# Kernel tuning notes

Hardware: AMD Instinct MI355X
Metric: run time of the kernel (lower is better)

## Reference

```python
import jax, jax.numpy as jnp
import numpy as np

B, N, F, E, D = 2, 50000, 128, 800000, 4


def setup_inputs() -> dict:
    key = jax.random.key(0)
    ks = jax.random.split(key, 6)
    X = jax.random.normal(ks[0], (B, N, F), dtype=jnp.float32)
    u_val = jax.random.normal(ks[1], (E, D), dtype=jnp.float32)
    u_rows = jax.random.randint(ks[2], (E,), 0, N, dtype=jnp.int32)
    u_cols = jax.random.randint(ks[3], (E,), 0, N, dtype=jnp.int32)
    mu = jax.random.uniform(ks[4], (1, D), minval=-0.05, maxval=0.05, dtype=jnp.float32)
    # sigma kept away from 0 so sigma^2 in the denominator is numerically sane
    sigma = jax.random.uniform(ks[5], (1, D), minval=0.5, maxval=1.5, dtype=jnp.float32)
    return {"X": X, "u_val": u_val, "u_rows": u_rows, "u_cols": u_cols,
            "mu": mu, "sigma": sigma, "u_shape": N}


def reference(X, u_val, u_rows, u_cols, mu, sigma, u_shape):
    n = u_shape  # python int, static
    # per-edge Gaussian kernel log-weight: -0.5 * sum_d (u-mu)^2 / (sigma^2+eps)
    w = -0.5 * jnp.sum(jnp.square(u_val - mu) / (jnp.square(sigma) + 1e-14), axis=1)  # [E]
    # sparse (segment) softmax over rows == tf.sparse.softmax on reordered SparseTensor
    m = jax.ops.segment_max(w, u_rows, num_segments=n)          # [N]
    e = jnp.exp(w - m[u_rows])                                  # [E]
    s = jax.ops.segment_sum(e, u_rows, num_segments=n)          # [N]
    sm = e / s[u_rows]                                          # [E]
    # sparse-dense matmul: D[b,i,f] = sum_{edges e: row=i} sm_e * X[b, col_e, f]
    Xt = jnp.transpose(X, (1, 0, 2))                            # [N,B,F]
    msg = sm[:, None, None] * Xt[u_cols]                        # [E,B,F]
    Dn = jax.ops.segment_sum(msg, u_rows, num_segments=n)       # [N,B,F]
    return jnp.transpose(Dn, (1, 0, 2))                         # [B,N,F]
```

## Files before the change

kernel.cpp:

```cpp
#include <hip/hip_runtime.h>

constexpr int Bc = 2;
constexpr int Fc = 128;
constexpr int F4 = Fc / 4;
constexpr int ROWS_PER_BLOCK = 4;
constexpr int EPT = 8;
constexpr int BIN_EDGES = 256 * EPT;

typedef float vfloat4 __attribute__((ext_vector_type(4)));

__device__ __forceinline__ unsigned short f2bf(float f) {
    unsigned u = __float_as_uint(f);
    unsigned r = (u + 0x7FFFu + ((u >> 16) & 1u)) >> 16;
    return (unsigned short)r;
}
__device__ __forceinline__ float bf2f(unsigned short h) {
    return __uint_as_float(((unsigned)h) << 16);
}
__device__ __forceinline__ void nt_store4(float4 v, float4* p) {
    vfloat4 q = {v.x, v.y, v.z, v.w};
    __builtin_nontemporal_store(q, (vfloat4*)p);
}

__global__ __launch_bounds__(256) void prep_kernel(const float4* __restrict__ uval,
                                                   const float* __restrict__ mu,
                                                   const float* __restrict__ sigma,
                                                   const int* __restrict__ rows,
                                                   const int* __restrict__ cols,
                                                   int2* __restrict__ bucket_buf,
                                                   int* __restrict__ bucket_cursor,
                                                   const float4* __restrict__ X4,
                                                   ushort4* __restrict__ Xb,
                                                   int E, int N, int cap, int nbuk,
                                                   int nbin) {
    __shared__ int hist[256];
    __shared__ int excl[256];
    __shared__ int fill[256];
    __shared__ int chunkb[256];
    __shared__ int sh[256];
    __shared__ int2 staged[BIN_EDGES];

    int t = threadIdx.x;

    if (blockIdx.x >= nbin) {
        long idx = (long)(blockIdx.x - nbin) * 256 + t;
        long tot = (long)Bc * N * F4;
        if (idx < tot) {
            int b  = (int)(idx / ((long)N * F4));
            int nt_ = (int)(idx - (long)b * N * F4);
            int n  = nt_ >> 5;
            int f4 = nt_ & 31;
            float4 v = X4[(size_t)b * N * F4 + nt_];
            ushort4 o;
            o.x = f2bf(v.x); o.y = f2bf(v.y); o.z = f2bf(v.z); o.w = f2bf(v.w);
            Xb[(size_t)n * (Bc * F4) + b * F4 + f4] = o;
        }
        return;
    }

    hist[t] = 0;
    float m0 = mu[0], m1 = mu[1], m2 = mu[2], m3 = mu[3];
    float i0 = 1.0f / (sigma[0] * sigma[0] + 1e-14f);
    float i1 = 1.0f / (sigma[1] * sigma[1] + 1e-14f);
    float i2 = 1.0f / (sigma[2] * sigma[2] + 1e-14f);
    float i3 = 1.0f / (sigma[3] * sigma[3] + 1e-14f);
    __syncthreads();

    int e0 = blockIdx.x * BIN_EDGES;
    int meta_r[EPT];
    float ev_r[EPT];
    int buk_r[EPT];
    #pragma unroll
    for (int it = 0; it < EPT; ++it) {
        int e = e0 + it * 256 + t;
        if (e < E) {
            int r = rows[e];
            int c = cols[e];
            float4 u = uval[e];
            float d0 = u.x - m0, d1 = u.y - m1, d2 = u.z - m2, d3 = u.w - m3;
            float w = -0.5f * (d0 * d0 * i0 + d1 * d1 * i1 + d2 * d2 * i2 + d3 * d3 * i3);
            ev_r[it]   = expf(w);
            meta_r[it] = (r << 16) | c;
            buk_r[it]  = r >> 8;
            atomicAdd(&hist[buk_r[it]], 1);
        } else {
            buk_r[it] = -1;
        }
    }
    __syncthreads();

    int v = hist[t];
    sh[t] = v;
    __syncthreads();
    for (int off = 1; off < 256; off <<= 1) {
        int a = (t >= off) ? sh[t - off] : 0;
        __syncthreads();
        sh[t] += a;
        __syncthreads();
    }
    excl[t] = sh[t] - v;
    fill[t] = sh[t] - v;

    if (t < nbuk && v > 0) chunkb[t] = atomicAdd(&bucket_cursor[t], v);
    __syncthreads();

    #pragma unroll
    for (int it = 0; it < EPT; ++it) {
        if (buk_r[it] >= 0) {
            int rk = atomicAdd(&fill[buk_r[it]], 1);
            staged[rk] = make_int2(meta_r[it], __float_as_int(ev_r[it]));
        }
    }
    __syncthreads();

    int nst = min(BIN_EDGES, E - e0);
    for (int k = t; k < nst; k += 256) {
        int2 x = staged[k];
        int buk = ((unsigned)x.x) >> 24;
        int rel = chunkb[buk] + (k - excl[buk]);
        if (rel < cap)
            bucket_buf[(size_t)buk * cap + rel] = x;
    }
}

__global__ __launch_bounds__(256) void csr_kernel(const int2* __restrict__ bucket_buf,
                                                  const int* __restrict__ bucket_cursor,
                                                  int2* __restrict__ pairs,
                                                  int* __restrict__ rowstart,
                                                  int cap, int N, int nbuk) {
    __shared__ int hist[256];
    __shared__ int excl[256];
    __shared__ int cur[256];
    __shared__ int sh[256];
    int b = blockIdx.x;
    int t = threadIdx.x;

    int szt = (t < nbuk) ? min(bucket_cursor[t], cap) : 0;
    sh[t] = szt;
    __syncthreads();
    for (int off = 1; off < 256; off <<= 1) {
        int a = (t >= off) ? sh[t - off] : 0;
        __syncthreads();
        sh[t] += a;
        __syncthreads();
    }
    int cbase = (b == 0) ? 0 : sh[b - 1];
    int size  = min(bucket_cursor[b], cap);
    if (b == nbuk - 1 && t == 0) rowstart[N] = sh[nbuk - 1];
    __syncthreads();

    hist[t] = 0;
    __syncthreads();
    int base = b * cap;
    for (int k = t; k < size; k += 256) {
        unsigned m = (unsigned)bucket_buf[base + k].x;
        atomicAdd(&hist[(m >> 16) & 0xFF], 1);
    }
    __syncthreads();
    int v = hist[t];
    sh[t] = v;
    __syncthreads();
    for (int off = 1; off < 256; off <<= 1) {
        int a = (t >= off) ? sh[t - off] : 0;
        __syncthreads();
        sh[t] += a;
        __syncthreads();
    }
    excl[t] = sh[t] - v;
    cur[t]  = sh[t] - v;
    int row = b * 256 + t;
    if (row < N) rowstart[row] = cbase + excl[t];
    __syncthreads();
    for (int k = t; k < size; k += 256) {
        int2 x = bucket_buf[base + k];
        unsigned m = (unsigned)x.x;
        int rk = atomicAdd(&cur[(m >> 16) & 0xFF], 1);
        pairs[cbase + rk] = make_int2((int)(m & 0xFFFFu), x.y);
    }
}

__global__ __launch_bounds__(256) void spmm_bf16(const ushort4* __restrict__ Xb,
                                                 const int2* __restrict__ pairs,
                                                 const int* __restrict__ rowstart,
                                                 float4* __restrict__ out4, int N) {
    int lane = threadIdx.x & 63;
    int i = blockIdx.x * ROWS_PER_BLOCK + (threadIdx.x >> 6);
    if (i >= N) return;
    int start = rowstart[i];
    int end   = rowstart[i + 1];
    int len   = end - start;
    float4 acc = {0.f, 0.f, 0.f, 0.f};
    float sum = 0.f;
    for (int c = 0; c < len; c += 64) {
        int m = min(64, len - c);
        int2 myp = make_int2(0, 0);
        if (lane < m) myp = pairs[start + c + lane];
        for (int g = 0; g < m; g += 8) {
            int   colv[8];
            float evv[8];
            #pragma unroll
            for (int e = 0; e < 8; ++e) {
                colv[e] = __shfl(myp.x, g + e);
                evv[e]  = __int_as_float(__shfl(myp.y, g + e));
            }
            ushort4 xs[8];
            #pragma unroll
            for (int e = 0; e < 8; ++e)
                xs[e] = Xb[(size_t)colv[e] * 64 + lane];
            #pragma unroll
            for (int e = 0; e < 8; ++e) {
                float ev = evv[e];
                sum += ev;
                acc.x = fmaf(ev, bf2f(xs[e].x), acc.x);
                acc.y = fmaf(ev, bf2f(xs[e].y), acc.y);
                acc.z = fmaf(ev, bf2f(xs[e].z), acc.z);
                acc.w = fmaf(ev, bf2f(xs[e].w), acc.w);
            }
        }
    }
    if (len > 0) {
        float inv = 1.0f / sum;
        acc.x *= inv; acc.y *= inv; acc.z *= inv; acc.w *= inv;
    }
    int b  = lane >> 5;
    int f4 = lane & 31;
    nt_store4(acc, &out4[(size_t)b * N * F4 + (size_t)i * F4 + f4]);
}

__global__ __launch_bounds__(256) void spmm_f32(const float4* __restrict__ X4,
                                                const int2* __restrict__ pairs,
                                                const int* __restrict__ rowstart,
                                                float4* __restrict__ out4, int N) {
    int lane = threadIdx.x & 63;
    int i = blockIdx.x * ROWS_PER_BLOCK + (threadIdx.x >> 6);
    if (i >= N) return;
    int start = rowstart[i];
    int end   = rowstart[i + 1];
    int b  = lane >> 5;
    int f4 = lane & 31;
    float4 acc = {0.f, 0.f, 0.f, 0.f};
    float sum = 0.f;
    if (start < end) {
        int xbase = b * N * F4 + f4;
        for (int j = start; j < end; ++j) {
            int2 p = pairs[j];
            float ev = __int_as_float(p.y);
            sum += ev;
            float4 x = X4[xbase + (size_t)p.x * F4];
            acc.x = fmaf(ev, x.x, acc.x);
            acc.y = fmaf(ev, x.y, acc.y);
            acc.z = fmaf(ev, x.z, acc.z);
            acc.w = fmaf(ev, x.w, acc.w);
        }
        float inv = 1.0f / sum;
        acc.x *= inv; acc.y *= inv; acc.z *= inv; acc.w *= inv;
    }
    nt_store4(acc, &out4[(size_t)b * N * F4 + (size_t)i * F4 + f4]);
}

extern "C" void kernel_launch(void* const* d_in, const int* in_sizes, int n_in,
                              void* d_out, int out_size, void* d_ws, size_t ws_size,
                              hipStream_t stream) {
    const float* X      = (const float*)d_in[0];
    const float* u_val  = (const float*)d_in[1];
    const int*   u_rows = (const int*)d_in[2];
    const int*   u_cols = (const int*)d_in[3];
    const float* mu     = (const float*)d_in[4];
    const float* sigma  = (const float*)d_in[5];

    const int E = in_sizes[2];
    const int N = in_sizes[0] / (Bc * Fc);
    const int nbuk = (N + 255) >> 8;

    size_t off = 0;
    auto carve = [&](size_t bytes) -> char* {
        char* p = (char*)d_ws + off;
        off = (off + bytes + 255) & ~(size_t)255;
        return p;
    };
    int*  bucket_cursor = (int*)carve(256 * 4);
    int*  rowstart      = (int*)carve((size_t)(N + 1) * 4);
    int2* pairs         = (int2*)carve((size_t)E * 8);

    size_t xb_bytes = (size_t)N * Bc * Fc * 2;
    size_t avail    = (ws_size > off) ? (ws_size - off) : 0;
    int cap = 6144;
    size_t buck_bytes = (size_t)nbuk * cap * 8;
    if (buck_bytes + 512 > avail) {
        cap = (int)((avail - 512) / ((size_t)nbuk * 8));
        buck_bytes = (size_t)nbuk * cap * 8;
    }
    int2* bucket_buf = (int2*)carve(buck_bytes);
    bool use_bf16 = (off + xb_bytes) <= ws_size;
    ushort4* Xb = use_bf16 ? (ushort4*)carve(xb_bytes) : nullptr;

    hipMemsetAsync(bucket_cursor, 0, 256 * 4, stream);

    const int nbin  = (E + BIN_EDGES - 1) / BIN_EDGES;
    const int nconv = use_bf16 ? (int)(((long)Bc * N * F4 + 255) / 256) : 0;
    prep_kernel<<<nbin + nconv, 256, 0, stream>>>(
        (const float4*)u_val, mu, sigma, u_rows, u_cols,
        bucket_buf, bucket_cursor, (const float4*)X, Xb,
        E, N, cap, nbuk, nbin);
    csr_kernel<<<nbuk, 256, 0, stream>>>(bucket_buf, bucket_cursor,
                                         pairs, rowstart, cap, N, nbuk);
    if (use_bf16) {
        spmm_bf16<<<(N + ROWS_PER_BLOCK - 1) / ROWS_PER_BLOCK, 256, 0, stream>>>(
            Xb, pairs, rowstart, (float4*)d_out, N);
    } else {
        spmm_f32<<<(N + ROWS_PER_BLOCK - 1) / ROWS_PER_BLOCK, 256, 0, stream>>>(
            (const float4*)X, pairs, rowstart, (float4*)d_out, N);
    }
}
```

Baseline: 100.1 us.

## Widen bf16 gathers to 16B, use wave-shuffle scans, stage CSR pairs in LDS

The SpMM kernel now has each wavefront split into two halves that each gather a different edge's row as 16-byte bf16 vectors. The partial sums are combined with a cross-half shuffle at the end, which halves the number of gather instructions per edge pair. Block-wide scans in the prep and CSR kernels are replaced by a wave-shuffle scan with fewer barriers. The CSR kernel stages sorted pairs in LDS so that global writes are coalesced. Non-temporal loads are used for the streamed inputs. The trade-off is more registers and a 48KB LDS buffer in the CSR kernel, which may lower occupancy.

```diff
diff --git a/kernel.cpp b/kernel.cpp
--- a/kernel.cpp
+++ b/kernel.cpp
@@ -6,8 +6,10 @@
 constexpr int ROWS_PER_BLOCK = 4;
 constexpr int EPT = 8;
 constexpr int BIN_EDGES = 256 * EPT;
+constexpr int CAP_MAX = 6144;
 
 typedef float vfloat4 __attribute__((ext_vector_type(4)));
+typedef unsigned short ushort8v __attribute__((ext_vector_type(8)));
 
 __device__ __forceinline__ unsigned short f2bf(float f) {
     unsigned u = __float_as_uint(f);
@@ -20,6 +22,26 @@
 __device__ __forceinline__ void nt_store4(float4 v, float4* p) {
     vfloat4 q = {v.x, v.y, v.z, v.w};
     __builtin_nontemporal_store(q, (vfloat4*)p);
+}
+__device__ __forceinline__ float4 nt_load4(const float4* p) {
+    vfloat4 q = __builtin_nontemporal_load((const vfloat4*)p);
+    float4 r; r.x = q.x; r.y = q.y; r.z = q.z; r.w = q.w;
+    return r;
+}
+
+__device__ __forceinline__ int block_incl_scan256(int v, int* wsum, int t) {
+    int lane = t & 63, w = t >> 6;
+    #pragma unroll
+    for (int d = 1; d < 64; d <<= 1) {
+        int u = __shfl_up(v, d);
+        if (lane >= d) v += u;
+    }
+    if (lane == 63) wsum[w] = v;
+    __syncthreads();
+    int add = 0;
+    #pragma unroll
+    for (int i = 0; i < 3; ++i) if (i < w) add += wsum[i];
+    return v + add;
 }
 
 __global__ __launch_bounds__(256) void prep_kernel(const float4* __restrict__ uval,
@@ -37,7 +59,7 @@
     __shared__ int excl[256];
     __shared__ int fill[256];
     __shared__ int chunkb[256];
-    __shared__ int sh[256];
+    __shared__ int wsum[4];
     __shared__ int2 staged[BIN_EDGES];
 
     int t = threadIdx.x;
@@ -50,7 +72,7 @@
             int nt_ = (int)(idx - (long)b * N * F4);
             int n  = nt_ >> 5;
             int f4 = nt_ & 31;
-            float4 v = X4[(size_t)b * N * F4 + nt_];
+            float4 v = nt_load4(&X4[(size_t)b * N * F4 + nt_]);
             ushort4 o;
             o.x = f2bf(v.x); o.y = f2bf(v.y); o.z = f2bf(v.z); o.w = f2bf(v.w);
             Xb[(size_t)n * (Bc * F4) + b * F4 + f4] = o;
@@ -76,7 +98,7 @@
         if (e < E) {
             int r = rows[e];
             int c = cols[e];
-            float4 u = uval[e];
+            float4 u = nt_load4((const float4*)&uval[e]);
             float d0 = u.x - m0, d1 = u.y - m1, d2 = u.z - m2, d3 = u.w - m3;
             float w = -0.5f * (d0 * d0 * i0 + d1 * d1 * i1 + d2 * d2 * i2 + d3 * d3 * i3);
             ev_r[it]   = expf(w);
@@ -90,17 +112,10 @@
     __syncthreads();
 
     int v = hist[t];
-    sh[t] = v;
-    __syncthreads();
-    for (int off = 1; off < 256; off <<= 1) {
-        int a = (t >= off) ? sh[t - off] : 0;
-        __syncthreads();
-        sh[t] += a;
-        __syncthreads();
-    }
-    excl[t] = sh[t] - v;
-    fill[t] = sh[t] - v;
-
+    int incl = block_incl_scan256(v, wsum, t);
+    int ex = incl - v;
+    excl[t] = ex;
+    fill[t] = ex;
     if (t < nbuk && v > 0) chunkb[t] = atomicAdd(&bucket_cursor[t], v);
     __syncthreads();
 
@@ -128,103 +143,124 @@
                                                   int2* __restrict__ pairs,
                                                   int* __restrict__ rowstart,
                                                   int cap, int N, int nbuk) {
-    __shared__ int hist[256];
+    __shared__ int sh[256];
+    __shared__ int cur[256];
     __shared__ int excl[256];
-    __shared__ int cur[256];
-    __shared__ int sh[256];
+    __shared__ int wsum[4];
+    __shared__ int2 staged[CAP_MAX];
     int b = blockIdx.x;
     int t = threadIdx.x;
 
     int szt = (t < nbuk) ? min(bucket_cursor[t], cap) : 0;
-    sh[t] = szt;
-    __syncthreads();
-    for (int off = 1; off < 256; off <<= 1) {
-        int a = (t >= off) ? sh[t - off] : 0;
-        __syncthreads();
-        sh[t] += a;
-        __syncthreads();
-    }
+    int incl = block_incl_scan256(szt, wsum, t);
+    sh[t] = incl;
+    __syncthreads();
     int cbase = (b == 0) ? 0 : sh[b - 1];
     int size  = min(bucket_cursor[b], cap);
-    if (b == nbuk - 1 && t == 0) rowstart[N] = sh[nbuk - 1];
-    __syncthreads();
-
-    hist[t] = 0;
+    if (b == 0 && t == 0) rowstart[N] = sh[nbuk - 1];
+    __syncthreads();
+
+    cur[t] = 0;
     __syncthreads();
     int base = b * cap;
     for (int k = t; k < size; k += 256) {
         unsigned m = (unsigned)bucket_buf[base + k].x;
-        atomicAdd(&hist[(m >> 16) & 0xFF], 1);
-    }
-    __syncthreads();
-    int v = hist[t];
-    sh[t] = v;
-    __syncthreads();
-    for (int off = 1; off < 256; off <<= 1) {
-        int a = (t >= off) ? sh[t - off] : 0;
-        __syncthreads();
-        sh[t] += a;
-        __syncthreads();
-    }
-    excl[t] = sh[t] - v;
-    cur[t]  = sh[t] - v;
+        atomicAdd(&cur[(m >> 16) & 0xFF], 1);
+    }
+    __syncthreads();
+    int v = cur[t];
+    int incl2 = block_incl_scan256(v, wsum, t);
+    int ex = incl2 - v;
+    excl[t] = ex;
+    __syncthreads();
+    cur[t] = ex;
     int row = b * 256 + t;
-    if (row < N) rowstart[row] = cbase + excl[t];
-    __syncthreads();
+    if (row < N) rowstart[row] = cbase + ex;
+    __syncthreads();
+
     for (int k = t; k < size; k += 256) {
         int2 x = bucket_buf[base + k];
         unsigned m = (unsigned)x.x;
         int rk = atomicAdd(&cur[(m >> 16) & 0xFF], 1);
-        pairs[cbase + rk] = make_int2((int)(m & 0xFFFFu), x.y);
-    }
-}
-
-__global__ __launch_bounds__(256) void spmm_bf16(const ushort4* __restrict__ Xb,
+        staged[rk] = make_int2((int)(m & 0xFFFFu), x.y);
+    }
+    __syncthreads();
+    for (int k = t; k < size; k += 256) pairs[cbase + k] = staged[k];
+}
+
+__global__ __launch_bounds__(256) void spmm_bf16(const ushort8v* __restrict__ Xb8,
                                                  const int2* __restrict__ pairs,
                                                  const int* __restrict__ rowstart,
                                                  float4* __restrict__ out4, int N) {
     int lane = threadIdx.x & 63;
+    int half = lane >> 5;
+    int sub  = lane & 31;
     int i = blockIdx.x * ROWS_PER_BLOCK + (threadIdx.x >> 6);
     if (i >= N) return;
     int start = rowstart[i];
-    int end   = rowstart[i + 1];
-    int len   = end - start;
-    float4 acc = {0.f, 0.f, 0.f, 0.f};
+    int len   = rowstart[i + 1] - start;
+    float acc[8] = {0.f, 0.f, 0.f, 0.f, 0.f, 0.f, 0.f, 0.f};
     float sum = 0.f;
     for (int c = 0; c < len; c += 64) {
         int m = min(64, len - c);
         int2 myp = make_int2(0, 0);
         if (lane < m) myp = pairs[start + c + lane];
-        for (int g = 0; g < m; g += 8) {
-            int   colv[8];
-            float evv[8];
+        int mr = (m + 7) & ~7;
+        for (int g = 0; g < mr; g += 16) {
+            bool two = (g + 8 < mr);
+            float evA[4]; ushort8v xA[4];
             #pragma unroll
-            for (int e = 0; e < 8; ++e) {
-                colv[e] = __shfl(myp.x, g + e);
-                evv[e]  = __int_as_float(__shfl(myp.y, g + e));
+            for (int q = 0; q < 4; ++q) {
+                int src = g + 2 * q + half;
+                int col = __shfl(myp.x, src);
+                evA[q]  = __int_as_float(__shfl(myp.y, src));
+                xA[q]   = Xb8[(size_t)col * 32 + sub];
             }
-            ushort4 xs[8];
+            float evB[4]; ushort8v xB[4];
+            if (two) {
+                #pragma unroll
+                for (int q = 0; q < 4; ++q) {
+                    int src = g + 8 + 2 * q + half;
+                    int col = __shfl(myp.x, src);
+                    evB[q]  = __int_as_float(__shfl(myp.y, src));
+                    xB[q]   = Xb8[(size_t)col * 32 + sub];
+                }
+            }
             #pragma unroll
-            for (int e = 0; e < 8; ++e)
-                xs[e] = Xb[(size_t)colv[e] * 64 + lane];
-            #pragma unroll
-            for (int e = 0; e < 8; ++e) {
-                float ev = evv[e];
-                sum += ev;
-                acc.x = fmaf(ev, bf2f(xs[e].x), acc.x);
-                acc.y = fmaf(ev, bf2f(xs[e].y), acc.y);
-                acc.z = fmaf(ev, bf2f(xs[e].z), acc.z);
-                acc.w = fmaf(ev, bf2f(xs[e].w), acc.w);
+            for (int q = 0; q < 4; ++q) {
+                float ev = evA[q]; sum += ev;
+                #pragma unroll
+                for (int k = 0; k < 8; ++k)
+                    acc[k] = fmaf(ev, bf2f(xA[q][k]), acc[k]);
             }
-        }
-    }
+            if (two) {
+                #pragma unroll
+                for (int q = 0; q < 4; ++q) {
+                    float ev = evB[q]; sum += ev;
+                    #pragma unroll
+                    for (int k = 0; k < 8; ++k)
+                        acc[k] = fmaf(ev, bf2f(xB[q][k]), acc[k]);
+                }
+            }
+        }
+    }
+    sum += __shfl_xor(sum, 32);
+    #pragma unroll
+    for (int k = 0; k < 8; ++k) acc[k] += __shfl_xor(acc[k], 32);
     if (len > 0) {
         float inv = 1.0f / sum;
-        acc.x *= inv; acc.y *= inv; acc.z *= inv; acc.w *= inv;
-    }
-    int b  = lane >> 5;
-    int f4 = lane & 31;
-    nt_store4(acc, &out4[(size_t)b * N * F4 + (size_t)i * F4 + f4]);
+        #pragma unroll
+        for (int k = 0; k < 8; ++k) acc[k] *= inv;
+    }
+    float4 o;
+    o.x = half ? acc[4] : acc[0];
+    o.y = half ? acc[5] : acc[1];
+    o.z = half ? acc[6] : acc[2];
+    o.w = half ? acc[7] : acc[3];
+    int f  = sub * 8 + half * 4;
+    int bb = f >> 7;
+    int f4 = (f & 127) >> 2;
+    nt_store4(o, &out4[(size_t)bb * N * F4 + (size_t)i * F4 + f4]);
 }
 
 __global__ __launch_bounds__(256) void spmm_f32(const float4* __restrict__ X4,
@@ -284,7 +320,7 @@
 
     size_t xb_bytes = (size_t)N * Bc * Fc * 2;
     size_t avail    = (ws_size > off) ? (ws_size - off) : 0;
-    int cap = 6144;
+    int cap = CAP_MAX;
     size_t buck_bytes = (size_t)nbuk * cap * 8;
     if (buck_bytes + 512 > avail) {
         cap = (int)((avail - 512) / ((size_t)nbuk * 8));
@@ -306,7 +342,7 @@
                                          pairs, rowstart, cap, N, nbuk);
     if (use_bf16) {
         spmm_bf16<<<(N + ROWS_PER_BLOCK - 1) / ROWS_PER_BLOCK, 256, 0, stream>>>(
-            Xb, pairs, rowstart, (float4*)d_out, N);
+            (const ushort8v*)Xb, pairs, rowstart, (float4*)d_out, N);
     } else {
         spmm_f32<<<(N + ROWS_PER_BLOCK - 1) / ROWS_PER_BLOCK, 256, 0, stream>>>(
             (const float4*)X, pairs, rowstart, (float4*)d_out, N);
```

After: 104.7 us. +4.6%, slower.
